# Kernel optimization log

Hardware: AMD Instinct MI355X
Metric: run time of the kernel (lower is better)

## Reference

```python
import jax, jax.numpy as jnp
import numpy as np

M, K, CH = 4, 256, 256
D = CH // M  # per-group dim = 64


def _conv(x, w, b, stride=2):
    # x: [N,C,H,W], w: [O,I,kh,kw]
    y = jax.lax.conv_general_dilated(
        x, w, window_strides=(stride, stride), padding='SAME',
        dimension_numbers=('NCHW', 'OIHW', 'NCHW'))
    return y + b[None, :, None, None]


def _encoder(x, w1, b1, w2, b2, w3, b3, w4, b4):
    x = jax.nn.gelu(_conv(x, w1, b1))
    x = jax.nn.gelu(_conv(x, w2, b2))
    x = jax.nn.gelu(_conv(x, w3, b3))
    return _conv(x, w4, b4)


def setup_inputs() -> dict:
    key = jax.random.key(0)
    ks = jax.random.split(key, 12)
    x = jax.random.uniform(ks[0], (16, 3, 256, 256), jnp.float32)

    def w(k, shape, fan_in):
        return jax.random.normal(k, shape, jnp.float32) * (1.0 / np.sqrt(fan_in))

    w1 = w(ks[1], (64, 3, 3, 3), 3 * 9);    b1 = jnp.zeros((64,), jnp.float32)
    w2 = w(ks[2], (128, 64, 3, 3), 64 * 9); b2 = jnp.zeros((128,), jnp.float32)
    w3 = w(ks[3], (256, 128, 3, 3), 128 * 9); b3 = jnp.zeros((256,), jnp.float32)
    w4 = w(ks[4], (CH, 256, 3, 3), 256 * 9); b4 = jnp.zeros((CH,), jnp.float32)
    codebook = w(ks[5], (M, K, D), D)
    wq = w(ks[6], (M, D, D), D)
    wk = w(ks[7], (M, D, D), D)
    return dict(x=x, w1=w1, b1=b1, w2=w2, b2=b2, w3=w3, b3=b3, w4=w4, b4=b4,
                codebook=codebook, wq=wq, wk=wk)


def reference(x, w1, b1, w2, b2, w3, b3, w4, b4, codebook, wq, wk):
    x = (x - 0.5) / 0.5
    n, c, h, w = x.shape  # c == 3 here, so the c==1 expand branch is skipped
    hPad = max(0, 32 - h)
    wPad = max(0, 32 - w)
    if hPad or wPad:
        x = jnp.pad(x, ((0, 0), (0, 0), (0, hPad), (0, wPad)))
    latent = _encoder(x, w1, b1, w2, b2, w3, b3, w4, b4)  # [n, CH, h/16, w/16]
    n2, _, hh, ww = latent.shape
    q = latent.transpose(0, 2, 3, 1).reshape(n2, hh, ww, M, D)
    q = jnp.einsum('nhwmd,mcd->nhwmc', q, wq)            # per-group query proj
    kproj = jnp.einsum('mkd,mcd->mkc', codebook, wk)     # per-group key proj
    scores = jnp.einsum('nhwmd,mkd->nhwmk', q, kproj)    # [n,hh,ww,m,k]
    code = jnp.argmax(scores, axis=-1).astype(jnp.uint8)
    return code, jnp.array([h, w], dtype=jnp.int32)
```

## Files before the change

kernel.cpp:

```cpp
#include <hip/hip_runtime.h>
#include <math.h>


typedef _Float16 half8 __attribute__((ext_vector_type(8)));
typedef float floatx4 __attribute__((ext_vector_type(4)));
typedef unsigned int u32;
typedef unsigned short u16;

__device__ __forceinline__ float gelu_tanh(float x) {
    float x3 = x * x * x;
    float t = 1.5957691216057308f * x + 0.07135481627333636f * x3;
    return x / (1.0f + __expf(-t));
}

__device__ __forceinline__ u32 pack_split(float v) {
    _Float16 h = (_Float16)v;
    _Float16 l = (_Float16)((v - (float)h) * 4096.0f);
    union { _Float16 f; u16 s; } a, b;
    a.f = h; b.f = l;
    return (u32)a.s | ((u32)b.s << 16);
}

template <int Ci, int Co>
__global__ void prep_w(const float* __restrict__ W, _Float16* __restrict__ dH,
                       _Float16* __restrict__ dL) {
    constexpr int KC = Ci / 32, NTg = Co / 16;
    int lin = blockIdx.x * 256 + threadIdx.x;
    if (lin >= 9 * KC * NTg * 64) return;
    int l = lin & 63;
    int q = lin >> 6;
    int nt = q % NTg; q /= NTg;
    int kc = q % KC;
    int tap = q / KC;
    int co = nt * 16 + (l & 15);
    int ci0 = kc * 32 + ((l >> 4) << 3);
#pragma unroll
    for (int j = 0; j < 8; ++j) {
        float v = W[((size_t)co * Ci + ci0 + j) * 9 + tap];
        _Float16 h = (_Float16)v;
        _Float16 lo = (_Float16)((v - (float)h) * 4096.0f);
        dH[(size_t)lin * 8 + j] = h;
        dL[(size_t)lin * 8 + j] = lo;
    }
}

__launch_bounds__(256)
__global__ void conv1_k(const float* __restrict__ x, const float* __restrict__ w,
                        const float* __restrict__ bias, u32* __restrict__ out) {
    __shared__ float win[17 * 260];
    __shared__ float wsh[27 * 64];
    const int t = threadIdx.x;
    const int tx = t & 15, ty = (t >> 4) & 7, cz = t >> 7;
    int bx = blockIdx.x;
    const int cg = bx & 3;
    const int oyt = (bx >> 2) & 15;
    const int n = bx >> 6;
    const int co0 = cg * 16 + cz * 8;
    const int oy = oyt * 8 + ty;
    const int ox0 = tx * 8;
    const int iy0 = oyt * 16;

    for (int e = t; e < 27 * 64; e += 256) {
        int co = e & 63, ct = e >> 6;
        wsh[ct * 64 + co] = w[co * 27 + ct];
    }

    float acc[8][8];
#pragma unroll
    for (int c = 0; c < 8; ++c)
#pragma unroll
        for (int p = 0; p < 8; ++p) acc[c][p] = 0.0f;

    for (int ci = 0; ci < 3; ++ci) {
        __syncthreads();
        for (int e = t; e < 17 * 260; e += 256) {
            int r = e / 260, c = e - r * 260;
            int iy = iy0 + r;
            float v = 0.0f;
            if (c < 256 && iy < 256)
                v = 2.0f * x[((size_t)(n * 3 + ci) * 256 + iy) * 256 + c] - 1.0f;
            win[e] = v;
        }
        __syncthreads();

#pragma unroll
        for (int ky = 0; ky < 3; ++ky) {
            const float* rowp = &win[(2 * ty + ky) * 260 + 16 * tx];
            float rv[20];
#pragma unroll
            for (int q = 0; q < 5; ++q) {
                float4 v4 = *(const float4*)(rowp + 4 * q);
                rv[4 * q + 0] = v4.x; rv[4 * q + 1] = v4.y;
                rv[4 * q + 2] = v4.z; rv[4 * q + 3] = v4.w;
            }
#pragma unroll
            for (int kx = 0; kx < 3; ++kx) {
                const float* wp = &wsh[(ci * 9 + ky * 3 + kx) * 64 + co0];
                float wv[8];
#pragma unroll
                for (int q = 0; q < 2; ++q) {
                    float4 v4 = *(const float4*)(wp + 4 * q);
                    wv[4 * q + 0] = v4.x; wv[4 * q + 1] = v4.y;
                    wv[4 * q + 2] = v4.z; wv[4 * q + 3] = v4.w;
                }
#pragma unroll
                for (int c = 0; c < 8; ++c)
#pragma unroll
                    for (int p = 0; p < 8; ++p)
                        acc[c][p] += rv[2 * p + kx] * wv[c];
            }
        }
    }

    float bj[8];
#pragma unroll
    for (int c = 0; c < 8; ++c) bj[c] = bias[co0 + c];
#pragma unroll
    for (int p = 0; p < 8; ++p) {
        int ox = ox0 + p;
        size_t base = ((size_t)(n * 128 + oy) * 128 + ox) * 64 + co0;
        uint4 s0, s1;
        s0.x = pack_split(gelu_tanh(acc[0][p] + bj[0]));
        s0.y = pack_split(gelu_tanh(acc[1][p] + bj[1]));
        s0.z = pack_split(gelu_tanh(acc[2][p] + bj[2]));
        s0.w = pack_split(gelu_tanh(acc[3][p] + bj[3]));
        s1.x = pack_split(gelu_tanh(acc[4][p] + bj[4]));
        s1.y = pack_split(gelu_tanh(acc[5][p] + bj[5]));
        s1.z = pack_split(gelu_tanh(acc[6][p] + bj[6]));
        s1.w = pack_split(gelu_tanh(acc[7][p] + bj[7]));
        *(uint4*)&out[base] = s0;
        *(uint4*)&out[base + 4] = s1;
    }
}

template <int Ci, int Co, int Hi, int Wi, bool GELU, bool SPLIT>
__launch_bounds__(512)
__global__ void conv_mfma(const u32* __restrict__ in, const _Float16* __restrict__ WbH,
                          const _Float16* __restrict__ WbL, const float* __restrict__ bias,
                          void* __restrict__ outp) {
    constexpr int Ho = Hi / 2, Wo = Wi / 2;
    constexpr int KC = Ci / 32, NTg = Co / 16;
    constexpr int OYT = Ho / 4, OXT = Wo / 16, CGT = Co / 128;
    constexpr int WC = 33, CIBP = 40;
    __shared__ _Float16 AH[9 * WC * CIBP], AL[9 * WC * CIBP];

    const int t = threadIdx.x, l = t & 63, wid = t >> 6;
    const int wm = wid >> 2, wn = wid & 3;
    int bx = blockIdx.x;
    const int cg = bx % CGT;  bx /= CGT;
    const int oxt = bx % OXT; bx /= OXT;
    const int oyt = bx % OYT; bx /= OYT;
    const int n = bx;
    const int oy0 = oyt * 4, ox0 = oxt * 16, co0 = cg * 128, nt0 = co0 >> 4;
    const int iy0 = oy0 * 2, ix0 = ox0 * 2;

    floatx4 aM[2][2], aX[2][2];
    floatx4 zz = {0.0f, 0.0f, 0.0f, 0.0f};
#pragma unroll
    for (int a = 0; a < 2; ++a)
#pragma unroll
        for (int b = 0; b < 2; ++b) { aM[a][b] = zz; aX[a][b] = zz; }

    const int bfrag = (wn * 2) * 512 + l * 8;

    for (int kc = 0; kc < KC; ++kc) {
        __syncthreads();
        for (int e = t; e < 9 * WC * 4; e += 512) {
            int og = e & 3, px = e >> 2;
            int r = px / WC, cx = px - r * WC;
            int iy = iy0 + r, ix = ix0 + cx;
            union { float4 f4[2]; u32 u[8]; } buf;
            if (iy < Hi && ix < Wi) {
                const float4* g = (const float4*)(in + (((size_t)(n * Hi + iy) * Wi + ix) * Ci + kc * 32 + og * 8));
                buf.f4[0] = g[0]; buf.f4[1] = g[1];
            } else {
#pragma unroll
                for (int k2 = 0; k2 < 8; ++k2) buf.u[k2] = 0;
            }
            union { float4 f4; u16 s[8]; } hh, ll;
#pragma unroll
            for (int k2 = 0; k2 < 8; ++k2) {
                hh.s[k2] = (u16)buf.u[k2];
                ll.s[k2] = (u16)(buf.u[k2] >> 16);
            }
            int off = px * CIBP + og * 8;
            *(float4*)&AH[off] = hh.f4;
            *(float4*)&AL[off] = ll.f4;
        }
        __syncthreads();

#pragma unroll
        for (int tap = 0; tap < 9; ++tap) {
            const size_t src = ((size_t)(tap * KC + kc) * NTg + nt0) * 512 + bfrag;
            half8 bh[2], bl[2];
#pragma unroll
            for (int b = 0; b < 2; ++b) {
                bh[b] = *(const half8*)&WbH[src + b * 512];
                bl[b] = *(const half8*)&WbL[src + b * 512];
            }
            const int ky = tap / 3, kx = tap - ky * 3;
#pragma unroll
            for (int a = 0; a < 2; ++a) {
                int mt = wm * 2 + a;
                int off = ((2 * mt + ky) * WC + 2 * (l & 15) + kx) * CIBP + (l >> 4) * 8;
                half8 ah = *(half8*)&AH[off];
                half8 al = *(half8*)&AL[off];
#pragma unroll
                for (int b = 0; b < 2; ++b) {
                    aM[a][b] = __builtin_amdgcn_mfma_f32_16x16x32_f16(ah, bh[b], aM[a][b], 0, 0, 0);
                    aX[a][b] = __builtin_amdgcn_mfma_f32_16x16x32_f16(ah, bl[b], aX[a][b], 0, 0, 0);
                    aX[a][b] = __builtin_amdgcn_mfma_f32_16x16x32_f16(al, bh[b], aX[a][b], 0, 0, 0);
                }
            }
        }
    }

#pragma unroll
    for (int a = 0; a < 2; ++a) {
        int oy = oy0 + wm * 2 + a;
#pragma unroll
        for (int b = 0; b < 2; ++b) {
            int co = co0 + (wn * 2 + b) * 16 + (l & 15);
            float bj = bias[co];
#pragma unroll
            for (int r = 0; r < 4; ++r) {
                int ox = ox0 + (l >> 4) * 4 + r;
                float v = aM[a][b][r] + aX[a][b][r] * (1.0f / 4096.0f) + bj;
                if (GELU) v = gelu_tanh(v);
                size_t oidx = ((size_t)(n * Ho + oy) * Wo + ox) * Co + co;
                if (SPLIT) ((u32*)outp)[oidx] = pack_split(v);
                else       ((float*)outp)[oidx] = v;
            }
        }
    }
}

__global__ void kproj_kernel(const float* __restrict__ cb,
                             const float* __restrict__ wk,
                             float* __restrict__ kp) {
    int m = blockIdx.x >> 8;
    int k = blockIdx.x & 255;
    int c = threadIdx.x;
    const float* cbp = cb + (size_t)(m * 256 + k) * 64;
    const float* wkp = wk + (size_t)(m * 64 + c) * 64;
    float acc = 0.0f;
#pragma unroll 8
    for (int d = 0; d < 64; ++d) acc += cbp[d] * wkp[d];
    kp[(size_t)(m * 256 + k) * 64 + c] = acc;
}

__global__ void m_kernel(const float* __restrict__ wq,
                         const float* __restrict__ kp,
                         float* __restrict__ M) {
    int m = blockIdx.x >> 8;
    int k = blockIdx.x & 255;
    int d = threadIdx.x;
    const float* kpp = &kp[(size_t)(m * 256 + k) * 64];
    const float* wqp = &wq[(size_t)m * 64 * 64 + d];
    float acc = 0.0f;
#pragma unroll 8
    for (int c = 0; c < 64; ++c) acc += wqp[c * 64] * kpp[c];
    M[((size_t)(m * 256 + k)) * 64 + d] = acc;
}

__launch_bounds__(256)
__global__ void head_kernel(const float* __restrict__ latent,
                            const float* __restrict__ M,
                            int* __restrict__ out) {
    __shared__ float rs[256];
    __shared__ int rk[256];
    const int t = threadIdx.x;
    const int px = t & 15, m = (t >> 4) & 3, kq = t >> 6;
    const int pix = blockIdx.x * 16 + px;

    float4 lr[16];
    const float4* lp = (const float4*)&latent[(size_t)pix * 256 + m * 64];
#pragma unroll
    for (int d = 0; d < 16; ++d) lr[d] = lp[d];

    float best = -INFINITY;
    int bestk = 0;
    const float4* Mp = (const float4*)&M[(size_t)((m * 256 + kq * 64)) * 64];
    for (int kk = 0; kk < 64; ++kk) {
        float s0 = 0.0f, s1 = 0.0f, s2 = 0.0f, s3 = 0.0f;
#pragma unroll
        for (int d = 0; d < 16; ++d) {
            float4 mv = Mp[kk * 16 + d];
            s0 += lr[d].x * mv.x; s1 += lr[d].y * mv.y;
            s2 += lr[d].z * mv.z; s3 += lr[d].w * mv.w;
        }
        float s = (s0 + s1) + (s2 + s3);
        if (s > best) { best = s; bestk = kq * 64 + kk; }
    }
    rs[t] = best; rk[t] = bestk;
    __syncthreads();
    if (kq == 0) {
#pragma unroll
        for (int q = 1; q < 4; ++q) {
            float sv = rs[t + 64 * q];
            int kv = rk[t + 64 * q];
            if (sv > best || (sv == best && kv < bestk)) { best = sv; bestk = kv; }
        }
        out[pix * 4 + m] = bestk;
    }
    if (blockIdx.x == 0 && t == 0) { out[16384] = 256; out[16385] = 256; }
}

extern "C" void kernel_launch(void* const* d_in, const int* in_sizes, int n_in,
                              void* d_out, int out_size, void* d_ws, size_t ws_size,
                              hipStream_t stream) {
    const float* x  = (const float*)d_in[0];
    const float* w1 = (const float*)d_in[1];  const float* b1 = (const float*)d_in[2];
    const float* w2 = (const float*)d_in[3];  const float* b2 = (const float*)d_in[4];
    const float* w3 = (const float*)d_in[5];  const float* b3 = (const float*)d_in[6];
    const float* w4 = (const float*)d_in[7];  const float* b4 = (const float*)d_in[8];
    const float* cb = (const float*)d_in[9];
    const float* wq = (const float*)d_in[10];
    const float* wk = (const float*)d_in[11];
    int* out = (int*)d_out;

    char* ws = (char*)d_ws;
    u32*   buf1 = (u32*)ws;
    u32*   buf2 = (u32*)(ws + 67108864);
    u32*   buf3 = (u32*)(ws + 100663296);
    float* buf4 = (float*)(ws + 117440512);
    float* kp   = (float*)(ws + 121634816);
    float* Mbuf = (float*)(ws + 121634816 + 262144);

    _Float16* w2H = (_Float16*)(ws + 100663296);
    _Float16* w2L = w2H + 9 * 2 * 8 * 512;
    _Float16* w3H = (_Float16*)ws;
    _Float16* w3L = w3H + 9 * 4 * 16 * 512;
    _Float16* w4H = w3L + 9 * 4 * 16 * 512;
    _Float16* w4L = w4H + 9 * 8 * 16 * 512;

    prep_w<64, 128><<<36, 256, 0, stream>>>(w2, w2H, w2L);
    conv1_k<<<1024, 256, 0, stream>>>(x, w1, b1, buf1);
    conv_mfma<64, 128, 128, 128, true, true><<<1024, 512, 0, stream>>>(buf1, w2H, w2L, b2, buf2);
    prep_w<128, 256><<<144, 256, 0, stream>>>(w3, w3H, w3L);
    prep_w<256, 256><<<288, 256, 0, stream>>>(w4, w4H, w4L);
    conv_mfma<128, 256, 64, 64, true, true><<<512, 512, 0, stream>>>(buf2, w3H, w3L, b3, buf3);
    kproj_kernel<<<4 * 256, 64, 0, stream>>>(cb, wk, kp);
    m_kernel<<<4 * 256, 64, 0, stream>>>(wq, kp, Mbuf);
    conv_mfma<256, 256, 32, 32, false, false><<<128, 512, 0, stream>>>(buf3, w4H, w4L, b4, buf4);
    head_kernel<<<256, 256, 0, stream>>>(buf4, Mbuf, out);
}
```

Measured before the change: 307.3 us.

## Split conv1 into 8 channel groups with fewer accumulators and vectorized input loads

The first convolution kernel now has each block compute 8 output channels instead of 16, with 4 channels per thread instead of 8. The grid doubles to 2048 blocks and per-block weight staging shrinks to only that block's channels. The input window is loaded with float4 reads instead of scalar ones. The aim is fewer registers per thread, higher occupancy and cheaper staging, at the cost of loading the input window twice as often across blocks.

```diff
diff --git a/kernel.cpp b/kernel.cpp
--- a/kernel.cpp
+++ b/kernel.cpp
@@ -48,38 +48,41 @@
 __global__ void conv1_k(const float* __restrict__ x, const float* __restrict__ w,
                         const float* __restrict__ bias, u32* __restrict__ out) {
     __shared__ float win[17 * 260];
-    __shared__ float wsh[27 * 64];
+    __shared__ float wsh[27 * 8];
     const int t = threadIdx.x;
     const int tx = t & 15, ty = (t >> 4) & 7, cz = t >> 7;
     int bx = blockIdx.x;
-    const int cg = bx & 3;
-    const int oyt = (bx >> 2) & 15;
-    const int n = bx >> 6;
-    const int co0 = cg * 16 + cz * 8;
+    const int cg = bx & 7;
+    const int oyt = (bx >> 3) & 15;
+    const int n = bx >> 7;
+    const int co0 = cg * 8 + cz * 4;
     const int oy = oyt * 8 + ty;
     const int ox0 = tx * 8;
     const int iy0 = oyt * 16;
 
-    for (int e = t; e < 27 * 64; e += 256) {
-        int co = e & 63, ct = e >> 6;
-        wsh[ct * 64 + co] = w[co * 27 + ct];
-    }
-
-    float acc[8][8];
-#pragma unroll
-    for (int c = 0; c < 8; ++c)
+    for (int e = t; e < 27 * 8; e += 256) {
+        int co = e & 7, ct = e >> 3;
+        wsh[ct * 8 + co] = w[(cg * 8 + co) * 27 + ct];
+    }
+
+    float acc[4][8];
+#pragma unroll
+    for (int c = 0; c < 4; ++c)
 #pragma unroll
         for (int p = 0; p < 8; ++p) acc[c][p] = 0.0f;
 
     for (int ci = 0; ci < 3; ++ci) {
         __syncthreads();
-        for (int e = t; e < 17 * 260; e += 256) {
-            int r = e / 260, c = e - r * 260;
+        for (int e = t; e < 17 * 65; e += 256) {
+            int r = e / 65, c4 = (e - r * 65) * 4;
             int iy = iy0 + r;
-            float v = 0.0f;
-            if (c < 256 && iy < 256)
-                v = 2.0f * x[((size_t)(n * 3 + ci) * 256 + iy) * 256 + c] - 1.0f;
-            win[e] = v;
+            float4 v = {0.0f, 0.0f, 0.0f, 0.0f};
+            if (c4 < 256 && iy < 256) {
+                float4 g = *(const float4*)&x[((size_t)(n * 3 + ci) * 256 + iy) * 256 + c4];
+                v.x = 2.0f * g.x - 1.0f; v.y = 2.0f * g.y - 1.0f;
+                v.z = 2.0f * g.z - 1.0f; v.w = 2.0f * g.w - 1.0f;
+            }
+            *(float4*)&win[r * 260 + c4] = v;
         }
         __syncthreads();
 
@@ -95,16 +98,10 @@
             }
 #pragma unroll
             for (int kx = 0; kx < 3; ++kx) {
-                const float* wp = &wsh[(ci * 9 + ky * 3 + kx) * 64 + co0];
-                float wv[8];
-#pragma unroll
-                for (int q = 0; q < 2; ++q) {
-                    float4 v4 = *(const float4*)(wp + 4 * q);
-                    wv[4 * q + 0] = v4.x; wv[4 * q + 1] = v4.y;
-                    wv[4 * q + 2] = v4.z; wv[4 * q + 3] = v4.w;
-                }
-#pragma unroll
-                for (int c = 0; c < 8; ++c)
+                float4 wv4 = *(const float4*)&wsh[(ci * 9 + ky * 3 + kx) * 8 + cz * 4];
+                float wv[4] = {wv4.x, wv4.y, wv4.z, wv4.w};
+#pragma unroll
+                for (int c = 0; c < 4; ++c)
 #pragma unroll
                     for (int p = 0; p < 8; ++p)
                         acc[c][p] += rv[2 * p + kx] * wv[c];
@@ -112,24 +109,19 @@
         }
     }
 
-    float bj[8];
-#pragma unroll
-    for (int c = 0; c < 8; ++c) bj[c] = bias[co0 + c];
+    float bj[4];
+#pragma unroll
+    for (int c = 0; c < 4; ++c) bj[c] = bias[co0 + c];
 #pragma unroll
     for (int p = 0; p < 8; ++p) {
         int ox = ox0 + p;
         size_t base = ((size_t)(n * 128 + oy) * 128 + ox) * 64 + co0;
-        uint4 s0, s1;
+        uint4 s0;
         s0.x = pack_split(gelu_tanh(acc[0][p] + bj[0]));
         s0.y = pack_split(gelu_tanh(acc[1][p] + bj[1]));
         s0.z = pack_split(gelu_tanh(acc[2][p] + bj[2]));
         s0.w = pack_split(gelu_tanh(acc[3][p] + bj[3]));
-        s1.x = pack_split(gelu_tanh(acc[4][p] + bj[4]));
-        s1.y = pack_split(gelu_tanh(acc[5][p] + bj[5]));
-        s1.z = pack_split(gelu_tanh(acc[6][p] + bj[6]));
-        s1.w = pack_split(gelu_tanh(acc[7][p] + bj[7]));
         *(uint4*)&out[base] = s0;
-        *(uint4*)&out[base + 4] = s1;
     }
 }
 
@@ -335,7 +327,7 @@
     _Float16* w4L = w4H + 9 * 8 * 16 * 512;
 
     prep_w<64, 128><<<36, 256, 0, stream>>>(w2, w2H, w2L);
-    conv1_k<<<1024, 256, 0, stream>>>(x, w1, b1, buf1);
+    conv1_k<<<2048, 256, 0, stream>>>(x, w1, b1, buf1);
     conv_mfma<64, 128, 128, 128, true, true><<<1024, 512, 0, stream>>>(buf1, w2H, w2L, b2, buf2);
     prep_w<128, 256><<<144, 256, 0, stream>>>(w3, w3H, w3L);
     prep_w<256, 256><<<288, 256, 0, stream>>>(w4, w4H, w4L);
```

Result: slower. 330.6 us (+7.6%).

## Restructure conv1 to read input directly from global memory, drop LDS input staging

Applied to the files above, without the earlier changes.

The first convolution no longer stages a 17-row input window in shared memory with two barriers per input channel. Each thread now loads its 9 input values straight from global memory and computes 16 output channels by 4 output pixels instead of 8 by 8. Shared memory holds only the 16-channel weight slice for the block, and launch bounds request 4 blocks per SM to raise occupancy. In exchange, input rows are re-read from global/cache by the four channel-group blocks and by neighbouring threads, and the per-output-pixel register reuse is lower.

```diff
diff --git a/kernel.cpp b/kernel.cpp
--- a/kernel.cpp
+++ b/kernel.cpp
@@ -44,92 +44,87 @@
     }
 }
 
-__launch_bounds__(256)
+__launch_bounds__(256, 4)
 __global__ void conv1_k(const float* __restrict__ x, const float* __restrict__ w,
                         const float* __restrict__ bias, u32* __restrict__ out) {
-    __shared__ float win[17 * 260];
-    __shared__ float wsh[27 * 64];
+    __shared__ float wsh[27 * 16];
     const int t = threadIdx.x;
-    const int tx = t & 15, ty = (t >> 4) & 7, cz = t >> 7;
+    const int tx = t & 31, ty = t >> 5;
     int bx = blockIdx.x;
     const int cg = bx & 3;
     const int oyt = (bx >> 2) & 15;
     const int n = bx >> 6;
-    const int co0 = cg * 16 + cz * 8;
+    const int co0 = cg * 16;
     const int oy = oyt * 8 + ty;
-    const int ox0 = tx * 8;
-    const int iy0 = oyt * 16;
-
-    for (int e = t; e < 27 * 64; e += 256) {
-        int co = e & 63, ct = e >> 6;
-        wsh[ct * 64 + co] = w[co * 27 + ct];
-    }
-
-    float acc[8][8];
-#pragma unroll
-    for (int c = 0; c < 8; ++c)
-#pragma unroll
-        for (int p = 0; p < 8; ++p) acc[c][p] = 0.0f;
-
+    const int ox0 = tx * 4;
+
+    for (int e = t; e < 27 * 16; e += 256) {
+        int co = e & 15, ct = e >> 4;
+        wsh[e] = w[(co0 + co) * 27 + ct];
+    }
+    __syncthreads();
+
+    float acc[16][4];
+#pragma unroll
+    for (int c = 0; c < 16; ++c)
+#pragma unroll
+        for (int p = 0; p < 4; ++p) acc[c][p] = 0.0f;
+
+    const float* xin = x + (size_t)n * 3 * 256 * 256;
+#pragma unroll
     for (int ci = 0; ci < 3; ++ci) {
-        __syncthreads();
-        for (int e = t; e < 17 * 260; e += 256) {
-            int r = e / 260, c = e - r * 260;
-            int iy = iy0 + r;
-            float v = 0.0f;
-            if (c < 256 && iy < 256)
-                v = 2.0f * x[((size_t)(n * 3 + ci) * 256 + iy) * 256 + c] - 1.0f;
-            win[e] = v;
-        }
-        __syncthreads();
-
 #pragma unroll
         for (int ky = 0; ky < 3; ++ky) {
-            const float* rowp = &win[(2 * ty + ky) * 260 + 16 * tx];
-            float rv[20];
-#pragma unroll
-            for (int q = 0; q < 5; ++q) {
-                float4 v4 = *(const float4*)(rowp + 4 * q);
-                rv[4 * q + 0] = v4.x; rv[4 * q + 1] = v4.y;
-                rv[4 * q + 2] = v4.z; rv[4 * q + 3] = v4.w;
+            const int iy = 2 * oy + ky;
+            float rv[9];
+            if (iy < 256) {
+                const float* rp = xin + ((size_t)ci * 256 + iy) * 256 + 8 * tx;
+                float4 a = *(const float4*)rp;
+                float4 b = *(const float4*)(rp + 4);
+                rv[0] = 2.0f * a.x - 1.0f; rv[1] = 2.0f * a.y - 1.0f;
+                rv[2] = 2.0f * a.z - 1.0f; rv[3] = 2.0f * a.w - 1.0f;
+                rv[4] = 2.0f * b.x - 1.0f; rv[5] = 2.0f * b.y - 1.0f;
+                rv[6] = 2.0f * b.z - 1.0f; rv[7] = 2.0f * b.w - 1.0f;
+                rv[8] = (tx < 31) ? 2.0f * rp[8] - 1.0f : 0.0f;
+            } else {
+#pragma unroll
+                for (int i = 0; i < 9; ++i) rv[i] = 0.0f;
             }
 #pragma unroll
             for (int kx = 0; kx < 3; ++kx) {
-                const float* wp = &wsh[(ci * 9 + ky * 3 + kx) * 64 + co0];
-                float wv[8];
-#pragma unroll
-                for (int q = 0; q < 2; ++q) {
+                const float* wp = &wsh[(ci * 9 + ky * 3 + kx) * 16];
+                float wv[16];
+#pragma unroll
+                for (int q = 0; q < 4; ++q) {
                     float4 v4 = *(const float4*)(wp + 4 * q);
                     wv[4 * q + 0] = v4.x; wv[4 * q + 1] = v4.y;
                     wv[4 * q + 2] = v4.z; wv[4 * q + 3] = v4.w;
                 }
 #pragma unroll
-                for (int c = 0; c < 8; ++c)
-#pragma unroll
-                    for (int p = 0; p < 8; ++p)
+                for (int c = 0; c < 16; ++c)
+#pragma unroll
+                    for (int p = 0; p < 4; ++p)
                         acc[c][p] += rv[2 * p + kx] * wv[c];
             }
         }
     }
 
-    float bj[8];
-#pragma unroll
-    for (int c = 0; c < 8; ++c) bj[c] = bias[co0 + c];
-#pragma unroll
-    for (int p = 0; p < 8; ++p) {
+    float bj[16];
+#pragma unroll
+    for (int c = 0; c < 16; ++c) bj[c] = bias[co0 + c];
+#pragma unroll
+    for (int p = 0; p < 4; ++p) {
         int ox = ox0 + p;
         size_t base = ((size_t)(n * 128 + oy) * 128 + ox) * 64 + co0;
-        uint4 s0, s1;
-        s0.x = pack_split(gelu_tanh(acc[0][p] + bj[0]));
-        s0.y = pack_split(gelu_tanh(acc[1][p] + bj[1]));
-        s0.z = pack_split(gelu_tanh(acc[2][p] + bj[2]));
-        s0.w = pack_split(gelu_tanh(acc[3][p] + bj[3]));
-        s1.x = pack_split(gelu_tanh(acc[4][p] + bj[4]));
-        s1.y = pack_split(gelu_tanh(acc[5][p] + bj[5]));
-        s1.z = pack_split(gelu_tanh(acc[6][p] + bj[6]));
-        s1.w = pack_split(gelu_tanh(acc[7][p] + bj[7]));
-        *(uint4*)&out[base] = s0;
-        *(uint4*)&out[base + 4] = s1;
+#pragma unroll
+        for (int cq = 0; cq < 4; ++cq) {
+            uint4 s0;
+            s0.x = pack_split(gelu_tanh(acc[4 * cq + 0][p] + bj[4 * cq + 0]));
+            s0.y = pack_split(gelu_tanh(acc[4 * cq + 1][p] + bj[4 * cq + 1]));
+            s0.z = pack_split(gelu_tanh(acc[4 * cq + 2][p] + bj[4 * cq + 2]));
+            s0.w = pack_split(gelu_tanh(acc[4 * cq + 3][p] + bj[4 * cq + 3]));
+            *(uint4*)&out[base + 4 * cq] = s0;
+        }
     }
 }
 
```

New measurement: 595.3 us. 1.94x slower.
